# Optimization experiments

Measured on AMD Instinct MI355X. Metric: run time of the kernel, lower is better.

Reference implementation:

```python
import jax, jax.numpy as jnp
import numpy as np

DROPOUT_P = 0.5


def normalize_adj(A):
    # A_tilda = A + I ; A_hat = D^-0.5 A_tilda D^-0.5
    # The torch code does this with diag_embed + two bmm (O(N^3));
    # mathematically it is row/col broadcasting (O(N^2)).
    B, N, _ = A.shape
    A_tilda = A + jnp.eye(N, dtype=A.dtype)
    d_inv_sqrt = jnp.sum(A_tilda, axis=2) ** -0.5          # [B, N]
    return d_inv_sqrt[:, :, None] * A_tilda * d_inv_sqrt[:, None, :]


def gcn_layer(X, A_hat, W, b):
    # standard Kipf GCN layer: A_hat @ (X @ W) + b
    return jnp.einsum('bnm,bmd->bnd', A_hat, X @ W) + b


def setup_inputs() -> dict:
    key = jax.random.key(0)
    ks = jax.random.split(key, 6)
    B, N, Din, H, C = 8, 2048, 64, 64, 16
    X = jax.random.normal(ks[0], (B, N, Din), dtype=jnp.float32)
    A = jax.random.uniform(ks[1], (B, N, N), dtype=jnp.float32)
    W1 = jax.random.normal(ks[2], (Din, H), dtype=jnp.float32) * (1.0 / np.sqrt(Din))
    b1 = jax.random.normal(ks[3], (H,), dtype=jnp.float32) * 0.01
    W2 = jax.random.normal(ks[4], (H, C), dtype=jnp.float32) * (1.0 / np.sqrt(H))
    b2 = jax.random.normal(ks[5], (C,), dtype=jnp.float32) * 0.01
    return {"X": X, "A": A, "W1": W1, "b1": b1, "W2": W2, "b2": b2}


def reference(X, A, W1, b1, W2, b2):
    A_hat = normalize_adj(A)
    h = jax.nn.relu(gcn_layer(X, A_hat, W1, b1))
    # F.dropout default training=True -> apply dropout with a fixed key
    keep = jax.random.bernoulli(jax.random.key(42), 1.0 - DROPOUT_P, h.shape)
    h = jnp.where(keep, h / (1.0 - DROPOUT_P), 0.0).astype(h.dtype)
    return gcn_layer(h, A_hat, W2, b2)
```

## Files before the change

### kernel.cpp

```cpp
#include <hip/hip_runtime.h>

#define BN 16384
#define NN 2048
#define DD 64
#define CC 16
#define KS1 8
#define KS2 16

typedef short bf16x8 __attribute__((ext_vector_type(8)));
typedef float f32x4 __attribute__((ext_vector_type(4)));
typedef unsigned short u16x4 __attribute__((ext_vector_type(4)));

__device__ __forceinline__ f32x4 mfma16(bf16x8 a, bf16x8 b, f32x4 c) {
  return __builtin_amdgcn_mfma_f32_16x16x32_bf16(a, b, c, 0, 0, 0);
}
__device__ __forceinline__ unsigned short f2bf(float f) {
  unsigned u = __float_as_uint(f);
  return (unsigned short)((u + 0x7FFFu + ((u >> 16) & 1u)) >> 16);
}
__device__ __forceinline__ float bf2f(unsigned short h) {
  return __uint_as_float(((unsigned)h) << 16);
}

__device__ __forceinline__ unsigned tf_bits(unsigned i) {
  unsigned x0 = 0u;
  unsigned x1 = i;
  const unsigned k0 = 0u, k1 = 42u, k2 = 0x1BD11BDAu ^ 0u ^ 42u;
  x0 += k0; x1 += k1;
#define TFR(r) { x0 += x1; x1 = (x1 << (r)) | (x1 >> (32 - (r))); x1 ^= x0; }
  TFR(13) TFR(15) TFR(26) TFR(6)
  x0 += k1; x1 += k2 + 1u;
  TFR(17) TFR(29) TFR(16) TFR(24)
  x0 += k2; x1 += k0 + 2u;
  TFR(13) TFR(15) TFR(26) TFR(6)
  x0 += k0; x1 += k1 + 3u;
  TFR(17) TFR(29) TFR(16) TFR(24)
  x0 += k1; x1 += k2 + 4u;
  TFR(13) TFR(15) TFR(26) TFR(6)
  x0 += k2; x1 += k0 + 5u;
#undef TFR
  return x0 ^ x1;
}


__global__ __launch_bounds__(256) void k_zero(float* __restrict__ S)
{
  const f32x4 z = 0.f;
  ((f32x4*)S)[blockIdx.x * 256 + threadIdx.x] = z;
}

__global__ __launch_bounds__(256) void k_deg(const float* __restrict__ A,
    const float* __restrict__ X, const float* __restrict__ W1,
    float* __restrict__ dis, unsigned short* __restrict__ Abf,
    unsigned short* __restrict__ Y1s, unsigned short* __restrict__ Y1sT)
{
  const int w = threadIdx.x >> 6, lane = threadIdx.x & 63;
  const size_t row = (size_t)blockIdx.x * 4 + w;
  const float4* Arow = (const float4*)(A + row * NN);
  unsigned short* Brow = Abf + row * NN;
  float s = 0.f;
#pragma unroll
  for (int it = 0; it < 8; ++it) {
    float4 v = Arow[lane + 64 * it];
    s += (v.x + v.y) + (v.z + v.w);
    u16x4 p = { f2bf(v.x), f2bf(v.y), f2bf(v.z), f2bf(v.w) };
    *(u16x4*)(Brow + lane * 4 + it * 256) = p;
  }
#pragma unroll
  for (int m = 32; m; m >>= 1) s += __shfl_xor(s, m, 64);
  const float dv = 1.0f / sqrtf(s + 1.0f);
  if (lane == 0) dis[row] = dv;
  const float* Xr = X + row * DD;
  float acc = 0.f;
#pragma unroll
  for (int k = 0; k < DD; ++k) acc += Xr[k] * W1[k * DD + lane];
  const unsigned short yv = f2bf(dv * acc);
  Y1s[row * DD + lane] = yv;
  const int b = (int)(row >> 11), kr = (int)(row & (NN - 1));
  Y1sT[((size_t)b * DD + lane) * NN + kr] = yv;
}

__global__ __launch_bounds__(256, 4) void k_gemm1(const unsigned short* __restrict__ Abf,
    const unsigned short* __restrict__ Y1sT, float* __restrict__ S1)
{
  const int Mb = blockIdx.x >> 4;
  const int ns = (blockIdx.x >> 3) & 1;
  const int ks = blockIdx.x & 7;
  const int w = __builtin_amdgcn_readfirstlane((int)threadIdx.x >> 6);
  const int lane = threadIdx.x & 63;
  const int m15 = lane & 15, quad = lane >> 4;
  const int b = Mb >> 3;
  const int k0 = ks * 256 + quad * 8;
  const unsigned short* Ap[4];
#pragma unroll
  for (int m = 0; m < 4; ++m)
    Ap[m] = Abf + ((size_t)Mb * 256 + m * 64 + w * 16 + m15) * NN + k0;
  const unsigned short* Bp0 = Y1sT + ((size_t)b * DD + ns * 32 + m15) * NN + k0;
  const unsigned short* Bp1 = Bp0 + (size_t)16 * NN;
  const f32x4 zero = 0.f;
  f32x4 acc[4][2];
#pragma unroll
  for (int m = 0; m < 4; ++m) { acc[m][0] = zero; acc[m][1] = zero; }
  bf16x8 a[4], b0, b1;
#pragma unroll
  for (int m = 0; m < 4; ++m) a[m] = *(const bf16x8*)Ap[m];
  b0 = *(const bf16x8*)Bp0;
  b1 = *(const bf16x8*)Bp1;
#pragma unroll 1
  for (int kk = 0; kk < 8; ++kk) {
    const int off = (kk < 7) ? (kk + 1) * 32 : 0;
    bf16x8 na[4], nb0, nb1;
#pragma unroll
    for (int m = 0; m < 4; ++m) na[m] = *(const bf16x8*)(Ap[m] + off);
    nb0 = *(const bf16x8*)(Bp0 + off);
    nb1 = *(const bf16x8*)(Bp1 + off);
#pragma unroll
    for (int m = 0; m < 4; ++m) {
      acc[m][0] = mfma16(a[m], b0, acc[m][0]);
      acc[m][1] = mfma16(a[m], b1, acc[m][1]);
    }
#pragma unroll
    for (int m = 0; m < 4; ++m) a[m] = na[m];
    b0 = nb0; b1 = nb1;
  }
#pragma unroll
  for (int m = 0; m < 4; ++m)
#pragma unroll
    for (int t = 0; t < 2; ++t)
#pragma unroll
      for (int r = 0; r < 4; ++r)
        atomicAdd(&S1[((size_t)Mb * 256 + m * 64 + w * 16 + quad * 4 + r) * DD
                      + ns * 32 + t * 16 + m15], acc[m][t][r]);
}

__global__ __launch_bounds__(256) void k_epi1(const float* __restrict__ S1,
    const unsigned short* __restrict__ Y1s, const float* __restrict__ dis,
    const float* __restrict__ b1, const float* __restrict__ W2,
    unsigned short* __restrict__ Y2sT, float* __restrict__ S2)
{
  __shared__ float hs[16][65];
  __shared__ float W2l[DD * CC];
  const int tid = threadIdx.x;
  *(float4*)(W2l + tid * 4) = *(const float4*)(W2 + tid * 4);
  const int r0 = blockIdx.x * 16;
#pragma unroll
  for (int j = 0; j < 4; ++j) {
    const int e = tid + j * 256;
    const int rl = e >> 6, n = e & 63;
    const size_t row = (size_t)r0 + rl;
    const size_t o = row * DD + n;
    const float z = bf2f(Y1s[o]) + S1[o];
    float h = fmaxf(dis[row] * z + b1[n], 0.f);
    const unsigned bits = tf_bits((unsigned)o);
    hs[rl][n] = (bits >> 31) ? 0.f : (h + h);
  }
  __syncthreads();
  const int c = tid & 15, rl = tid >> 4;
  float s = 0.f;
#pragma unroll
  for (int k = 0; k < DD; ++k) s += hs[rl][k] * W2l[k * CC + c];
  const int row = r0 + rl;
  const int b = row >> 11, kr = row & (NN - 1);
  const float y2 = dis[row] * s;
  Y2sT[((size_t)b * CC + c) * NN + kr] = f2bf(y2);
  S2[(size_t)row * CC + c] = y2;
}

__global__ __launch_bounds__(256, 4) void k_gemm2(const unsigned short* __restrict__ Abf,
    const unsigned short* __restrict__ Y2sT, float* __restrict__ S2)
{
  const int Mb = blockIdx.x >> 4;
  const int ks = blockIdx.x & 15;
  const int w = __builtin_amdgcn_readfirstlane((int)threadIdx.x >> 6);
  const int lane = threadIdx.x & 63;
  const int m15 = lane & 15, quad = lane >> 4;
  const int b = Mb >> 3;
  const int k0 = ks * 128 + quad * 8;
  const unsigned short* Ap[4];
#pragma unroll
  for (int m = 0; m < 4; ++m)
    Ap[m] = Abf + ((size_t)Mb * 256 + m * 64 + w * 16 + m15) * NN + k0;
  const unsigned short* Bp = Y2sT + ((size_t)b * CC + m15) * NN + k0;
  const f32x4 zero = 0.f;
  f32x4 acc[4];
#pragma unroll
  for (int m = 0; m < 4; ++m) acc[m] = zero;
  bf16x8 a[4], bb;
#pragma unroll
  for (int m = 0; m < 4; ++m) a[m] = *(const bf16x8*)Ap[m];
  bb = *(const bf16x8*)Bp;
#pragma unroll 1
  for (int kk = 0; kk < 4; ++kk) {
    const int off = (kk < 3) ? (kk + 1) * 32 : 0;
    bf16x8 na[4], nbb;
#pragma unroll
    for (int m = 0; m < 4; ++m) na[m] = *(const bf16x8*)(Ap[m] + off);
    nbb = *(const bf16x8*)(Bp + off);
#pragma unroll
    for (int m = 0; m < 4; ++m) acc[m] = mfma16(a[m], bb, acc[m]);
#pragma unroll
    for (int m = 0; m < 4; ++m) a[m] = na[m];
    bb = nbb;
  }
#pragma unroll
  for (int m = 0; m < 4; ++m)
#pragma unroll
    for (int r = 0; r < 4; ++r)
      atomicAdd(&S2[((size_t)Mb * 256 + m * 64 + w * 16 + quad * 4 + r) * CC + m15],
                acc[m][r]);
}

__global__ __launch_bounds__(256) void k_final(const float* __restrict__ S2,
    const float* __restrict__ dis, const float* __restrict__ b2,
    float* __restrict__ out)
{
  const int gid = blockIdx.x * 256 + threadIdx.x;
  const int r = gid >> 2, q = gid & 3;
  const size_t o = (size_t)r * CC + q * 4;
  const float4 s = *(const float4*)(S2 + o);
  const float dv = dis[r];
  const float4 bb = *(const float4*)(b2 + q * 4);
  float4 res;
  res.x = dv * s.x + bb.x;
  res.y = dv * s.y + bb.y;
  res.z = dv * s.z + bb.z;
  res.w = dv * s.w + bb.w;
  *(float4*)(out + o) = res;
}

#define FKS1 4
#define FKS2 16

__global__ __launch_bounds__(256) void d_deg_xw(const float* __restrict__ A,
    const float* __restrict__ X, const float* __restrict__ W1,
    float* __restrict__ dis, float* __restrict__ Y1s)
{
  const int w = threadIdx.x >> 6, lane = threadIdx.x & 63;
  const int row = __builtin_amdgcn_readfirstlane(blockIdx.x * 4 + w);
  const float4* Arow = (const float4*)(A + (size_t)row * NN);
  float s = 0.f;
#pragma unroll
  for (int it = 0; it < 8; ++it) {
    float4 v = Arow[lane + 64 * it];
    s += v.x + v.y + v.z + v.w;
  }
#pragma unroll
  for (int m = 32; m; m >>= 1) s += __shfl_xor(s, m, 64);
  const float dv = 1.0f / sqrtf(s + 1.0f);
  if (lane == 0) dis[row] = dv;
  const float* Xr = X + (size_t)row * DD;
  float acc = 0.f;
#pragma unroll
  for (int k = 0; k < DD; ++k) acc += Xr[k] * W1[k * DD + lane];
  Y1s[(size_t)row * DD + lane] = dv * acc;
}

__global__ __launch_bounds__(256) void d_gemm1(const float* __restrict__ A,
    const float* __restrict__ Y1s, float* __restrict__ Z1)
{
  const int rb = blockIdx.x >> 2, ks = blockIdx.x & (FKS1 - 1);
  const int lane = threadIdx.x & 63;
  const int c0 = __builtin_amdgcn_readfirstlane((threadIdx.x >> 6) << 4);
  const int row = rb * 64 + lane;
  const int batch = rb >> 5;
  const int KSEG = NN / FKS1;
  const float* Arow = A + (size_t)row * NN + ks * KSEG;
  const float* Yb = Y1s + (size_t)batch * NN * DD + c0;
  const int kbase = ks * KSEG;
  float acc[16];
#pragma unroll
  for (int c = 0; c < 16; ++c) acc[c] = 0.f;
  float4 a0 = *(const float4*)(Arow);
  float4 a1 = *(const float4*)(Arow + 4);
  float4 a2 = *(const float4*)(Arow + 8);
  float4 a3 = *(const float4*)(Arow + 12);
  for (int k = 0; k < KSEG; k += 16) {
    const int kn = (k + 16 < KSEG) ? (k + 16) : 0;
    float4 n0 = *(const float4*)(Arow + kn);
    float4 n1 = *(const float4*)(Arow + kn + 4);
    float4 n2 = *(const float4*)(Arow + kn + 8);
    float4 n3 = *(const float4*)(Arow + kn + 12);
    const float* y0 = Yb + (size_t)(kbase + k) * DD;
    const float av[16] = {a0.x, a0.y, a0.z, a0.w, a1.x, a1.y, a1.z, a1.w,
                          a2.x, a2.y, a2.z, a2.w, a3.x, a3.y, a3.z, a3.w};
#pragma unroll
    for (int j = 0; j < 16; ++j) {
      const float* yr = y0 + j * DD;
#pragma unroll
      for (int c = 0; c < 16; ++c) acc[c] += av[j] * yr[c];
    }
    a0 = n0; a1 = n1; a2 = n2; a3 = n3;
  }
  float* Zp = Z1 + ((size_t)ks * BN + row) * DD + c0;
#pragma unroll
  for (int c = 0; c < 16; c += 4) {
    float4 v; v.x = acc[c]; v.y = acc[c+1]; v.z = acc[c+2]; v.w = acc[c+3];
    *(float4*)(Zp + c) = v;
  }
}

__global__ __launch_bounds__(256) void d_epi1(const float* __restrict__ Z1,
    const float* __restrict__ Y1s, const float* __restrict__ dis,
    const float* __restrict__ b1, const float* __restrict__ W2,
    float* __restrict__ Y2s)
{
  __shared__ float W2l[DD * CC];
  __shared__ float hl[4][DD];
  const int tid = threadIdx.x;
  *(float4*)(W2l + tid * 4) = *(const float4*)(W2 + tid * 4);
  const int w = tid >> 6, lane = tid & 63;
  const int row = blockIdx.x * 4 + w;
  const size_t o = (size_t)row * DD + lane;
  float z = Y1s[o];
#pragma unroll
  for (int p = 0; p < FKS1; ++p) z += Z1[(size_t)p * BN * DD + o];
  const float dv = dis[row];
  float h = fmaxf(dv * z + b1[lane], 0.f);
  const unsigned bits = tf_bits((unsigned)o);
  h = (bits >> 31) ? 0.f : (h + h);
  hl[w][lane] = h;
  __syncthreads();
  const int wr = tid >> 6, l = tid & 63;
  const int c = l & 15, kq = l >> 4;
  float p = 0.f;
#pragma unroll
  for (int kk = 0; kk < 16; ++kk)
    p += hl[wr][kq * 16 + kk] * W2l[(kq * 16 + kk) * CC + c];
  p += __shfl_xor(p, 16, 64);
  p += __shfl_xor(p, 32, 64);
  if (l < 16) {
    const int rg = blockIdx.x * 4 + wr;
    Y2s[(size_t)rg * CC + c] = dis[rg] * p;
  }
}

__global__ __launch_bounds__(256) void d_gemm2(const float* __restrict__ A,
    const float* __restrict__ Y2s, float* __restrict__ Z2)
{
  const int rb = blockIdx.x >> 4, ks = blockIdx.x & (FKS2 - 1);
  const int row = rb * 256 + threadIdx.x;
  const int batch = rb >> 3;
  const int KSEG = NN / FKS2;
  const float* Arow = A + (size_t)row * NN + ks * KSEG;
  const float* Yb = Y2s + (size_t)batch * NN * CC;
  const int kbase = ks * KSEG;
  float acc[16];
#pragma unroll
  for (int c = 0; c < 16; ++c) acc[c] = 0.f;
  float4 a0 = *(const float4*)(Arow);
  float4 a1 = *(const float4*)(Arow + 4);
  for (int k = 0; k < KSEG; k += 8) {
    const int kn = (k + 8 < KSEG) ? (k + 8) : 0;
    float4 n0 = *(const float4*)(Arow + kn);
    float4 n1 = *(const float4*)(Arow + kn + 4);
    const float av[8] = {a0.x, a0.y, a0.z, a0.w, a1.x, a1.y, a1.z, a1.w};
#pragma unroll
    for (int j = 0; j < 8; ++j) {
      const float* yr = Yb + (size_t)(kbase + k + j) * CC;
#pragma unroll
      for (int c = 0; c < 16; ++c) acc[c] += av[j] * yr[c];
    }
    a0 = n0; a1 = n1;
  }
  float* Zp = Z2 + ((size_t)ks * BN + row) * CC;
#pragma unroll
  for (int c = 0; c < 16; c += 4) {
    float4 v; v.x = acc[c]; v.y = acc[c+1]; v.z = acc[c+2]; v.w = acc[c+3];
    *(float4*)(Zp + c) = v;
  }
}

__global__ __launch_bounds__(256) void d_final(const float* __restrict__ Z2,
    const float* __restrict__ Y2s, const float* __restrict__ dis,
    const float* __restrict__ b2, float* __restrict__ out)
{
  const int gid = blockIdx.x * 256 + threadIdx.x;
  const int r = gid >> 2, q = gid & 3;
  const size_t o = (size_t)r * CC + q * 4;
  float4 s = *(const float4*)(Y2s + o);
#pragma unroll
  for (int p = 0; p < FKS2; ++p) {
    const float4 zp = *(const float4*)(Z2 + (size_t)p * BN * CC + o);
    s.x += zp.x; s.y += zp.y; s.z += zp.z; s.w += zp.w;
  }
  const float dv = dis[r];
  const float4 bb = *(const float4*)(b2 + q * 4);
  float4 res;
  res.x = dv * s.x + bb.x;
  res.y = dv * s.y + bb.y;
  res.z = dv * s.z + bb.z;
  res.w = dv * s.w + bb.w;
  *(float4*)(out + o) = res;
}

extern "C" void kernel_launch(void* const* d_in, const int* in_sizes, int n_in,
                              void* d_out, int out_size, void* d_ws, size_t ws_size,
                              hipStream_t stream) {
  const float* X  = (const float*)d_in[0];
  const float* A  = (const float*)d_in[1];
  const float* W1 = (const float*)d_in[2];
  const float* b1 = (const float*)d_in[3];
  const float* W2 = (const float*)d_in[4];
  const float* b2 = (const float*)d_in[5];
  float* out = (float*)d_out;
  char* wsb = (char*)d_ws;

  const size_t NEED = 77135872;
  if (ws_size >= NEED) {
    unsigned short* Abf  = (unsigned short*)wsb;
    float*          S1   = (float*)(wsb + 67108864);
    float*          S2   = (float*)(wsb + 71303168);
    float*          dis  = (float*)(wsb + 72351744);
    unsigned short* Y1s  = (unsigned short*)(wsb + 72417280);
    unsigned short* Y1sT = (unsigned short*)(wsb + 74514432);
    unsigned short* Y2sT = (unsigned short*)(wsb + 76611584);

    k_zero <<<1280,    256, 0, stream>>>(S1);
    k_deg  <<<BN / 4,  256, 0, stream>>>(A, X, W1, dis, Abf, Y1s, Y1sT);
    k_gemm1<<<1024,    256, 0, stream>>>(Abf, Y1sT, S1);
    k_epi1 <<<BN / 16, 256, 0, stream>>>(S1, Y1s, dis, b1, W2, Y2sT, S2);
    k_gemm2<<<1024,    256, 0, stream>>>(Abf, Y2sT, S2);
    k_final<<<256,     256, 0, stream>>>(S2, dis, b2, out);
  } else {
    float* ws  = (float*)d_ws;
    float* dis = ws;
    float* Y1s = ws + 16384;
    float* Z1  = Y1s + (size_t)BN * DD;
    float* Z2  = Z1;
    float* Y2s = Z1 + (size_t)FKS1 * BN * DD;

    d_deg_xw<<<BN / 4,     256, 0, stream>>>(A, X, W1, dis, Y1s);
    d_gemm1 <<<256 * FKS1, 256, 0, stream>>>(A, Y1s, Z1);
    d_epi1  <<<BN / 4,     256, 0, stream>>>(Z1, Y1s, dis, b1, W2, Y2s);
    d_gemm2 <<<64 * FKS2,  256, 0, stream>>>(A, Y2s, Z2);
    d_final <<<256,        256, 0, stream>>>(Z2, Y2s, dis, b2, out);
  }
}
```

Baseline: 295.9 us.

## Replace split-K atomics with in-block LDS reduction and fuse epilogues into GEMMs

Both GEMMs now split K across the four waves of a block and combine the partial sums in shared memory, so the global float atomics go away. That also removes the zeroing kernel. The layer-1 ReLU, dropout and bias epilogue is fused into gemm1, which writes H in bf16. The final scale-and-bias is fused into gemm2, cutting the launch count from six to four. In exchange each block covers fewer rows (32 or 16), so A-tile reuse across output columns drops and gemm1 reads A twice, once per column half.

```diff
diff --git a/kernel.cpp b/kernel.cpp
--- a/kernel.cpp
+++ b/kernel.cpp
@@ -4,8 +4,6 @@
 #define NN 2048
 #define DD 64
 #define CC 16
-#define KS1 8
-#define KS2 16
 
 typedef short bf16x8 __attribute__((ext_vector_type(8)));
 typedef float f32x4 __attribute__((ext_vector_type(4)));
@@ -43,12 +41,6 @@
 }
 
 
-__global__ __launch_bounds__(256) void k_zero(float* __restrict__ S)
-{
-  const f32x4 z = 0.f;
-  ((f32x4*)S)[blockIdx.x * 256 + threadIdx.x] = z;
-}
-
 __global__ __launch_bounds__(256) void k_deg(const float* __restrict__ A,
     const float* __restrict__ X, const float* __restrict__ W1,
     float* __restrict__ dis, unsigned short* __restrict__ Abf,
@@ -80,79 +72,89 @@
   Y1sT[((size_t)b * DD + lane) * NN + kr] = yv;
 }
 
-__global__ __launch_bounds__(256, 4) void k_gemm1(const unsigned short* __restrict__ Abf,
-    const unsigned short* __restrict__ Y1sT, float* __restrict__ S1)
-{
-  const int Mb = blockIdx.x >> 4;
-  const int ns = (blockIdx.x >> 3) & 1;
-  const int ks = blockIdx.x & 7;
+__global__ __launch_bounds__(256, 4) void k_gemm1h(const unsigned short* __restrict__ Abf,
+    const unsigned short* __restrict__ Y1sT, const unsigned short* __restrict__ Y1s,
+    const float* __restrict__ dis, const float* __restrict__ b1,
+    unsigned short* __restrict__ Hbf)
+{
+  __shared__ float red[4][32][36];
+  const int Mb = blockIdx.x >> 1;
+  const int ns = blockIdx.x & 1;
   const int w = __builtin_amdgcn_readfirstlane((int)threadIdx.x >> 6);
   const int lane = threadIdx.x & 63;
   const int m15 = lane & 15, quad = lane >> 4;
-  const int b = Mb >> 3;
-  const int k0 = ks * 256 + quad * 8;
-  const unsigned short* Ap[4];
-#pragma unroll
-  for (int m = 0; m < 4; ++m)
-    Ap[m] = Abf + ((size_t)Mb * 256 + m * 64 + w * 16 + m15) * NN + k0;
+  const int b = Mb >> 6;
+  const int k0 = w * 512 + quad * 8;
+  const unsigned short* Ap0 = Abf + ((size_t)Mb * 32 + m15) * NN + k0;
+  const unsigned short* Ap1 = Ap0 + (size_t)16 * NN;
   const unsigned short* Bp0 = Y1sT + ((size_t)b * DD + ns * 32 + m15) * NN + k0;
   const unsigned short* Bp1 = Bp0 + (size_t)16 * NN;
   const f32x4 zero = 0.f;
-  f32x4 acc[4][2];
-#pragma unroll
-  for (int m = 0; m < 4; ++m) { acc[m][0] = zero; acc[m][1] = zero; }
-  bf16x8 a[4], b0, b1;
-#pragma unroll
-  for (int m = 0; m < 4; ++m) a[m] = *(const bf16x8*)Ap[m];
-  b0 = *(const bf16x8*)Bp0;
-  b1 = *(const bf16x8*)Bp1;
+  f32x4 acc[2][2];
+  acc[0][0] = zero; acc[0][1] = zero; acc[1][0] = zero; acc[1][1] = zero;
+  bf16x8 a0 = *(const bf16x8*)Ap0, a1 = *(const bf16x8*)Ap1;
+  bf16x8 b0 = *(const bf16x8*)Bp0, b1v = *(const bf16x8*)Bp1;
 #pragma unroll 1
-  for (int kk = 0; kk < 8; ++kk) {
-    const int off = (kk < 7) ? (kk + 1) * 32 : 0;
-    bf16x8 na[4], nb0, nb1;
-#pragma unroll
-    for (int m = 0; m < 4; ++m) na[m] = *(const bf16x8*)(Ap[m] + off);
-    nb0 = *(const bf16x8*)(Bp0 + off);
-    nb1 = *(const bf16x8*)(Bp1 + off);
-#pragma unroll
-    for (int m = 0; m < 4; ++m) {
-      acc[m][0] = mfma16(a[m], b0, acc[m][0]);
-      acc[m][1] = mfma16(a[m], b1, acc[m][1]);
-    }
-#pragma unroll
-    for (int m = 0; m < 4; ++m) a[m] = na[m];
-    b0 = nb0; b1 = nb1;
-  }
-#pragma unroll
-  for (int m = 0; m < 4; ++m)
-#pragma unroll
-    for (int t = 0; t < 2; ++t)
+  for (int kk = 0; kk < 16; ++kk) {
+    const int off = (kk < 15) ? (kk + 1) * 32 : 0;
+    bf16x8 na0 = *(const bf16x8*)(Ap0 + off);
+    bf16x8 na1 = *(const bf16x8*)(Ap1 + off);
+    bf16x8 nb0 = *(const bf16x8*)(Bp0 + off);
+    bf16x8 nb1 = *(const bf16x8*)(Bp1 + off);
+    acc[0][0] = mfma16(a0, b0, acc[0][0]);
+    acc[0][1] = mfma16(a0, b1v, acc[0][1]);
+    acc[1][0] = mfma16(a1, b0, acc[1][0]);
+    acc[1][1] = mfma16(a1, b1v, acc[1][1]);
+    a0 = na0; a1 = na1; b0 = nb0; b1v = nb1;
+  }
+#pragma unroll
+  for (int mi = 0; mi < 2; ++mi)
+#pragma unroll
+    for (int ni = 0; ni < 2; ++ni)
 #pragma unroll
       for (int r = 0; r < 4; ++r)
-        atomicAdd(&S1[((size_t)Mb * 256 + m * 64 + w * 16 + quad * 4 + r) * DD
-                      + ns * 32 + t * 16 + m15], acc[m][t][r]);
-}
-
-__global__ __launch_bounds__(256) void k_epi1(const float* __restrict__ S1,
-    const unsigned short* __restrict__ Y1s, const float* __restrict__ dis,
-    const float* __restrict__ b1, const float* __restrict__ W2,
-    unsigned short* __restrict__ Y2sT, float* __restrict__ S2)
-{
-  __shared__ float hs[16][65];
+        red[w][mi * 16 + quad * 4 + r][ni * 16 + m15] = acc[mi][ni][r];
+  __syncthreads();
+  const int tid = threadIdx.x;
+  const int rowl = tid >> 3, c0 = (tid & 7) * 4;
+  f32x4 sum = *(const f32x4*)&red[0][rowl][c0];
+  sum += *(const f32x4*)&red[1][rowl][c0];
+  sum += *(const f32x4*)&red[2][rowl][c0];
+  sum += *(const f32x4*)&red[3][rowl][c0];
+  const int grow = Mb * 32 + rowl;
+  const int gcol0 = ns * 32 + c0;
+  const u16x4 y1d = *(const u16x4*)(Y1s + (size_t)grow * DD + gcol0);
+  const float4 b1q = *(const float4*)(b1 + gcol0);
+  const float dv = dis[grow];
+  const unsigned o0 = (unsigned)grow * DD + gcol0;
+  u16x4 hq;
+#pragma unroll
+  for (int j = 0; j < 4; ++j) {
+    const float z = sum[j] + bf2f(y1d[j]);
+    const float bj = j == 0 ? b1q.x : j == 1 ? b1q.y : j == 2 ? b1q.z : b1q.w;
+    float h = fmaxf(dv * z + bj, 0.f);
+    const unsigned bits = tf_bits(o0 + j);
+    hq[j] = (bits >> 31) ? (unsigned short)0 : f2bf(h + h);
+  }
+  *(u16x4*)(Hbf + (size_t)grow * DD + gcol0) = hq;
+}
+
+__global__ __launch_bounds__(256) void k_epi1(const unsigned short* __restrict__ Hbf,
+    const float* __restrict__ dis, const float* __restrict__ W2,
+    unsigned short* __restrict__ Y2sT, float* __restrict__ S2d)
+{
+  __shared__ float hs[16][68];
   __shared__ float W2l[DD * CC];
   const int tid = threadIdx.x;
   *(float4*)(W2l + tid * 4) = *(const float4*)(W2 + tid * 4);
   const int r0 = blockIdx.x * 16;
-#pragma unroll
-  for (int j = 0; j < 4; ++j) {
-    const int e = tid + j * 256;
-    const int rl = e >> 6, n = e & 63;
-    const size_t row = (size_t)r0 + rl;
-    const size_t o = row * DD + n;
-    const float z = bf2f(Y1s[o]) + S1[o];
-    float h = fmaxf(dis[row] * z + b1[n], 0.f);
-    const unsigned bits = tf_bits((unsigned)o);
-    hs[rl][n] = (bits >> 31) ? 0.f : (h + h);
+  {
+    const int rl = tid >> 4, cl = (tid & 15) * 4;
+    const u16x4 hv = *(const u16x4*)(Hbf + ((size_t)r0 + rl) * DD + cl);
+    hs[rl][cl + 0] = bf2f(hv[0]);
+    hs[rl][cl + 1] = bf2f(hv[1]);
+    hs[rl][cl + 2] = bf2f(hv[2]);
+    hs[rl][cl + 3] = bf2f(hv[3]);
   }
   __syncthreads();
   const int c = tid & 15, rl = tid >> 4;
@@ -163,69 +165,46 @@
   const int b = row >> 11, kr = row & (NN - 1);
   const float y2 = dis[row] * s;
   Y2sT[((size_t)b * CC + c) * NN + kr] = f2bf(y2);
-  S2[(size_t)row * CC + c] = y2;
-}
-
-__global__ __launch_bounds__(256, 4) void k_gemm2(const unsigned short* __restrict__ Abf,
-    const unsigned short* __restrict__ Y2sT, float* __restrict__ S2)
-{
-  const int Mb = blockIdx.x >> 4;
-  const int ks = blockIdx.x & 15;
+  S2d[(size_t)row * CC + c] = y2;
+}
+
+__global__ __launch_bounds__(256, 4) void k_gemm2o(const unsigned short* __restrict__ Abf,
+    const unsigned short* __restrict__ Y2sT, const float* __restrict__ S2d,
+    const float* __restrict__ dis, const float* __restrict__ b2,
+    float* __restrict__ out)
+{
+  __shared__ float red[4][16][20];
+  const int Mb = blockIdx.x;
   const int w = __builtin_amdgcn_readfirstlane((int)threadIdx.x >> 6);
   const int lane = threadIdx.x & 63;
   const int m15 = lane & 15, quad = lane >> 4;
-  const int b = Mb >> 3;
-  const int k0 = ks * 128 + quad * 8;
-  const unsigned short* Ap[4];
-#pragma unroll
-  for (int m = 0; m < 4; ++m)
-    Ap[m] = Abf + ((size_t)Mb * 256 + m * 64 + w * 16 + m15) * NN + k0;
+  const int b = Mb >> 7;
+  const int k0 = w * 512 + quad * 8;
+  const unsigned short* Ap = Abf + ((size_t)Mb * 16 + m15) * NN + k0;
   const unsigned short* Bp = Y2sT + ((size_t)b * CC + m15) * NN + k0;
   const f32x4 zero = 0.f;
-  f32x4 acc[4];
-#pragma unroll
-  for (int m = 0; m < 4; ++m) acc[m] = zero;
-  bf16x8 a[4], bb;
-#pragma unroll
-  for (int m = 0; m < 4; ++m) a[m] = *(const bf16x8*)Ap[m];
-  bb = *(const bf16x8*)Bp;
+  f32x4 acc = zero;
+  bf16x8 a = *(const bf16x8*)Ap;
+  bf16x8 bb = *(const bf16x8*)Bp;
 #pragma unroll 1
-  for (int kk = 0; kk < 4; ++kk) {
-    const int off = (kk < 3) ? (kk + 1) * 32 : 0;
-    bf16x8 na[4], nbb;
-#pragma unroll
-    for (int m = 0; m < 4; ++m) na[m] = *(const bf16x8*)(Ap[m] + off);
-    nbb = *(const bf16x8*)(Bp + off);
-#pragma unroll
-    for (int m = 0; m < 4; ++m) acc[m] = mfma16(a[m], bb, acc[m]);
-#pragma unroll
-    for (int m = 0; m < 4; ++m) a[m] = na[m];
-    bb = nbb;
-  }
-#pragma unroll
-  for (int m = 0; m < 4; ++m)
-#pragma unroll
-    for (int r = 0; r < 4; ++r)
-      atomicAdd(&S2[((size_t)Mb * 256 + m * 64 + w * 16 + quad * 4 + r) * CC + m15],
-                acc[m][r]);
-}
-
-__global__ __launch_bounds__(256) void k_final(const float* __restrict__ S2,
-    const float* __restrict__ dis, const float* __restrict__ b2,
-    float* __restrict__ out)
-{
-  const int gid = blockIdx.x * 256 + threadIdx.x;
-  const int r = gid >> 2, q = gid & 3;
-  const size_t o = (size_t)r * CC + q * 4;
-  const float4 s = *(const float4*)(S2 + o);
-  const float dv = dis[r];
-  const float4 bb = *(const float4*)(b2 + q * 4);
-  float4 res;
-  res.x = dv * s.x + bb.x;
-  res.y = dv * s.y + bb.y;
-  res.z = dv * s.z + bb.z;
-  res.w = dv * s.w + bb.w;
-  *(float4*)(out + o) = res;
+  for (int kk = 0; kk < 16; ++kk) {
+    const int off = (kk < 15) ? (kk + 1) * 32 : 0;
+    bf16x8 na = *(const bf16x8*)(Ap + off);
+    bf16x8 nbb = *(const bf16x8*)(Bp + off);
+    acc = mfma16(a, bb, acc);
+    a = na; bb = nbb;
+  }
+#pragma unroll
+  for (int r = 0; r < 4; ++r)
+    red[w][quad * 4 + r][m15] = acc[r];
+  __syncthreads();
+  const int tid = threadIdx.x;
+  const int rowl = tid >> 4, c = tid & 15;
+  const float sum = red[0][rowl][c] + red[1][rowl][c]
+                  + red[2][rowl][c] + red[3][rowl][c];
+  const int grow = Mb * 16 + rowl;
+  out[(size_t)grow * CC + c] =
+      dis[grow] * (sum + S2d[(size_t)grow * CC + c]) + b2[c];
 }
 
 #define FKS1 4
@@ -405,22 +384,20 @@
   float* out = (float*)d_out;
   char* wsb = (char*)d_ws;
 
-  const size_t NEED = 77135872;
+  const size_t NEED = 75038720;
   if (ws_size >= NEED) {
     unsigned short* Abf  = (unsigned short*)wsb;
-    float*          S1   = (float*)(wsb + 67108864);
-    float*          S2   = (float*)(wsb + 71303168);
-    float*          dis  = (float*)(wsb + 72351744);
-    unsigned short* Y1s  = (unsigned short*)(wsb + 72417280);
-    unsigned short* Y1sT = (unsigned short*)(wsb + 74514432);
-    unsigned short* Y2sT = (unsigned short*)(wsb + 76611584);
-
-    k_zero <<<1280,    256, 0, stream>>>(S1);
-    k_deg  <<<BN / 4,  256, 0, stream>>>(A, X, W1, dis, Abf, Y1s, Y1sT);
-    k_gemm1<<<1024,    256, 0, stream>>>(Abf, Y1sT, S1);
-    k_epi1 <<<BN / 16, 256, 0, stream>>>(S1, Y1s, dis, b1, W2, Y2sT, S2);
-    k_gemm2<<<1024,    256, 0, stream>>>(Abf, Y2sT, S2);
-    k_final<<<256,     256, 0, stream>>>(S2, dis, b2, out);
+    unsigned short* Y1s  = (unsigned short*)(wsb + 67108864);
+    unsigned short* Y1sT = (unsigned short*)(wsb + 69206016);
+    unsigned short* Hbf  = (unsigned short*)(wsb + 71303168);
+    unsigned short* Y2sT = (unsigned short*)(wsb + 73400320);
+    float*          S2d  = (float*)(wsb + 73924608);
+    float*          dis  = (float*)(wsb + 74973184);
+
+    k_deg   <<<BN / 4, 256, 0, stream>>>(A, X, W1, dis, Abf, Y1s, Y1sT);
+    k_gemm1h<<<1024,   256, 0, stream>>>(Abf, Y1sT, Y1s, dis, b1, Hbf);
+    k_epi1  <<<1024,   256, 0, stream>>>(Hbf, dis, W2, Y2sT, S2d);
+    k_gemm2o<<<1024,   256, 0, stream>>>(Abf, Y2sT, S2d, dis, b2, out);
   } else {
     float* ws  = (float*)d_ws;
     float* dis = ws;
```

After: 270.6 us. -8.5%, faster.
